# Performance work log

Measured on AMD Instinct MI355X. Metric: run time of the kernel, lower is better.

## Reference

```python
import jax, jax.numpy as jnp
import numpy as np
from jax import lax

B, C_IN, L = 16, 2, 8192
D, H, NL = 256, 8, 4
DK = D // H
DFF = 2 * D
S = L // 8  # downsampled length = 1024
EPS = 1e-5


def _pe(seq, d):
    pos = jnp.arange(seq, dtype=jnp.float32)[:, None]
    div = jnp.exp(jnp.arange(0, d, 2, dtype=jnp.float32) * (-np.log(10000.0) / d))
    pe = jnp.zeros((seq, d), dtype=jnp.float32)
    pe = pe.at[:, 0::2].set(jnp.sin(pos * div))
    pe = pe.at[:, 1::2].set(jnp.cos(pos * div))
    return pe  # (seq, d)


def _layernorm(x, g, b):
    m = jnp.mean(x, axis=-1, keepdims=True)
    v = jnp.mean((x - m) ** 2, axis=-1, keepdims=True)
    return (x - m) * lax.rsqrt(v + EPS) * g + b


def setup_inputs() -> dict:
    key = jax.random.key(0)
    ks = jax.random.split(key, 20)
    sd = 0.02
    inp = {
        'x': jax.random.normal(ks[0], (B, C_IN, L), jnp.float32),
        'conv1_w': jax.random.normal(ks[1], (32, C_IN, 8), jnp.float32) * sd,
        'conv1_b': jnp.zeros((32,), jnp.float32),
        'conv2_w': jax.random.normal(ks[2], (D, 32, 4), jnp.float32) * sd,
        'conv2_b': jnp.zeros((D,), jnp.float32),
        'wq': jax.random.normal(ks[3], (NL, D, D), jnp.float32) * sd,
        'bq': jnp.zeros((NL, D), jnp.float32),
        'wk': jax.random.normal(ks[4], (NL, D, D), jnp.float32) * sd,
        'bk': jnp.zeros((NL, D), jnp.float32),
        'wv': jax.random.normal(ks[5], (NL, D, D), jnp.float32) * sd,
        'bv': jnp.zeros((NL, D), jnp.float32),
        'wo': jax.random.normal(ks[6], (NL, D, D), jnp.float32) * sd,
        'bo': jnp.zeros((NL, D), jnp.float32),
        'ln1_g': jnp.ones((NL, D), jnp.float32),
        'ln1_b': jnp.zeros((NL, D), jnp.float32),
        'ff_w1': jax.random.normal(ks[7], (NL, D, DFF), jnp.float32) * sd,
        'ff_b1': jnp.zeros((NL, DFF), jnp.float32),
        'ff_w2': jax.random.normal(ks[8], (NL, DFF, D), jnp.float32) * sd,
        'ff_b2': jnp.zeros((NL, D), jnp.float32),
        'ln2_g': jnp.ones((NL, D), jnp.float32),
        'ln2_b': jnp.zeros((NL, D), jnp.float32),
        'cls_w1': jax.random.normal(ks[9], (D, D // 2), jnp.float32) * sd,
        'cls_b1': jnp.zeros((D // 2,), jnp.float32),
        'cls_w2': jax.random.normal(ks[10], (D // 2, 1), jnp.float32) * sd,
        'cls_b2': jnp.zeros((1,), jnp.float32),
    }
    return inp


def reference(x, conv1_w, conv1_b, conv2_w, conv2_b,
              wq, bq, wk, bk, wv, bv, wo, bo,
              ln1_g, ln1_b, ff_w1, ff_b1, ff_w2, ff_b2, ln2_g, ln2_b,
              cls_w1, cls_b1, cls_w2, cls_b2):
    dn = ('NCH', 'OIH', 'NCH')
    # downsampler: conv(k8,s4,p2) -> relu -> conv(k4,s2,p1) -> relu
    h = lax.conv_general_dilated(x, conv1_w, (4,), [(2, 2)], dimension_numbers=dn)
    h = jax.nn.relu(h + conv1_b[None, :, None])
    h = lax.conv_general_dilated(h, conv2_w, (2,), [(1, 1)], dimension_numbers=dn)
    h = jax.nn.relu(h + conv2_b[None, :, None])
    h = h.transpose(0, 2, 1)  # (B, S, D)
    h = h + _pe(h.shape[1], D)[None]
    scale = 1.0 / np.sqrt(DK)
    for i in range(NL):
        # multi-head attention (explicit QK^T -> softmax -> V)
        q = (h @ wq[i] + bq[i]).reshape(B, S, H, DK)
        k = (h @ wk[i] + bk[i]).reshape(B, S, H, DK)
        v = (h @ wv[i] + bv[i]).reshape(B, S, H, DK)
        scores = jnp.einsum('bqhd,bkhd->bhqk', q, k) * scale
        attn = jax.nn.softmax(scores, axis=-1)
        ctx = jnp.einsum('bhqk,bkhd->bqhd', attn, v).reshape(B, S, D)
        h = _layernorm(h + ctx @ wo[i] + bo[i], ln1_g[i], ln1_b[i])
        ff = jax.nn.relu(h @ ff_w1[i] + ff_b1[i]) @ ff_w2[i] + ff_b2[i]
        h = _layernorm(h + ff, ln2_g[i], ln2_b[i])
    pooled = jnp.mean(h, axis=1)  # (B, D)
    logits = jax.nn.relu(pooled @ cls_w1 + cls_b1) @ cls_w2 + cls_b2
    return jax.nn.sigmoid(logits)  # (B, 1)
```

## Files before the change

### kernel.cpp

```cpp
#include <hip/hip_runtime.h>
#include <math.h>

typedef unsigned short u16;
typedef __attribute__((ext_vector_type(8))) short bf16x8;
typedef __attribute__((ext_vector_type(4))) float f32x4;
typedef __attribute__((ext_vector_type(16))) float f32x16;

#define B_ 16
#define L_ 8192
#define D_ 256
#define H_ 8
#define NL_ 4
#define DFF_ 512
#define S_ 1024
#define L1_ 2048
#define MROWS_ 16384

__device__ __forceinline__ u16 f2bf(float f) {
    unsigned u = __float_as_uint(f);
    unsigned r = (u + 0x7fffu + ((u >> 16) & 1u)) >> 16;
    return (u16)r;
}
__device__ __forceinline__ float fexp2(float x) {
    return __builtin_amdgcn_exp2f(x);
}
__device__ __forceinline__ unsigned cvtpk(float a, float b) {
    unsigned r;
    asm("v_cvt_pk_bf16_f32 %0, %1, %2" : "=v"(r) : "v"(a), "v"(b));
    return r;
}
__device__ __forceinline__ void pl32swap(unsigned& dst, unsigned& src) {
    asm volatile("v_permlane32_swap_b32 %0, %1" : "+v"(dst), "+v"(src));
}
__device__ __forceinline__ int swz16(int b) { return b ^ ((b >> 3) & 0x18); }

typedef __attribute__((address_space(1))) const void gvoid;
typedef __attribute__((address_space(3))) void lvoid;
__device__ __forceinline__ void gll16(const void* g, void* l) {
    __builtin_amdgcn_global_load_lds((gvoid*)g, (lvoid*)l, 16, 0, 0);
}
__device__ __forceinline__ void stage64(const u16* src, int ld, u16* lds, int tid) {
    gll16(src + (size_t)(tid >> 2) * ld + (tid & 3) * 8, lds + (tid >> 6) * 512);
}

__global__ __launch_bounds__(256) void conv1_im2col_kernel(const float* __restrict__ x,
                                                           const float* __restrict__ w,
                                                           const float* __restrict__ bias,
                                                           u16* __restrict__ A2) {
    int idx = blockIdx.x * 256 + threadIdx.x;
    int k = idx & 127, row = idx >> 7;
    int c = k >> 2, j = k & 3;
    int b = row >> 10, s = row & 1023;
    int p = s * 2 - 1 + j;
    float v = 0.f;
    if (p >= 0 && p < L1_) {
        float acc = bias[c];
        int base = p * 4 - 2;
#pragma unroll
        for (int ci = 0; ci < 2; ++ci) {
            const float* xr = x + ((size_t)(b * 2 + ci)) * L_;
            const float* wr = w + (c * 2 + ci) * 8;
#pragma unroll
            for (int jj = 0; jj < 8; ++jj) {
                int pos = base + jj;
                if (pos >= 0 && pos < L_) acc += xr[pos] * wr[jj];
            }
        }
        v = fmaxf(acc, 0.f);
    }
    A2[idx] = f2bf(v);
}

__global__ __launch_bounds__(256) void pack_all(const float* __restrict__ wq,
                                                const float* __restrict__ wk,
                                                const float* __restrict__ wv,
                                                const float* __restrict__ wo,
                                                const float* __restrict__ ff_w1,
                                                const float* __restrict__ ff_w2,
                                                const float* __restrict__ conv2_w,
                                                const float* __restrict__ bq,
                                                const float* __restrict__ bk,
                                                const float* __restrict__ bv,
                                                u16* __restrict__ qkvT, u16* __restrict__ woT,
                                                u16* __restrict__ ff1T, u16* __restrict__ ff2T,
                                                u16* __restrict__ w2cT,
                                                float* __restrict__ pe, float* __restrict__ bqkv,
                                                float* __restrict__ pooled, float qscale) {
    int id = blockIdx.x * 256 + threadIdx.x;
    if (id < 786432) {
        int l = id / 196608, j = id % 196608;
        int row = j >> 8, k = j & 255;
        const float* src; float sc = 1.f; int n;
        if (row < 256) { src = wq; n = row; sc = qscale; }
        else if (row < 512) { src = wk; n = row - 256; }
        else { src = wv; n = row - 512; }
        qkvT[id] = f2bf(src[((size_t)l * 256 + k) * 256 + n] * sc);
        return;
    }
    id -= 786432;
    if (id < 262144) {
        int l = id >> 16, j = id & 65535;
        int n = j >> 8, k = j & 255;
        woT[id] = f2bf(wo[((size_t)l * 256 + k) * 256 + n]);
        return;
    }
    id -= 262144;
    if (id < 524288) {
        int l = id >> 17, j = id & 131071;
        int n = j >> 8, k = j & 255;
        ff1T[id] = f2bf(ff_w1[((size_t)l * 256 + k) * 512 + n]);
        return;
    }
    id -= 524288;
    if (id < 524288) {
        int l = id >> 17, j = id & 131071;
        int n = j >> 9, k = j & 511;
        ff2T[id] = f2bf(ff_w2[((size_t)l * 512 + k) * 256 + n]);
        return;
    }
    id -= 524288;
    if (id < 32768) { w2cT[id] = f2bf(conv2_w[id]); return; }
    id -= 32768;
    if (id < 262144) {
        int s = id >> 8, d = id & 255;
        int i2 = d & ~1;
        float div = expf((float)i2 * (-9.210340371976184f / 256.f));
        float arg = (float)s * div;
        pe[id] = (d & 1) ? cosf(arg) : sinf(arg);
        return;
    }
    id -= 262144;
    if (id < 3072) {
        int l = id / 768, n = id % 768;
        const float* src = (n < 256) ? bq : (n < 512) ? bk : bv;
        float sc = (n < 256) ? qscale : 1.f;
        bqkv[id] = src[l * 256 + (n & 255)] * sc;
        return;
    }
    id -= 3072;
    if (id < 4096) pooled[id] = 0.f;
}

template <int EP>
__global__ __launch_bounds__(256) void mfma_gemm128(const u16* __restrict__ A, int lda,
                                                    const u16* __restrict__ WT,
                                                    const float* __restrict__ bias,
                                                    const float* __restrict__ pe,
                                                    float* __restrict__ hout,
                                                    u16* __restrict__ outB,
                                                    u16* __restrict__ ktout,
                                                    u16* __restrict__ vtout,
                                                    int N, int K) {
    __shared__ u16 Alds[128 * 32];
    __shared__ u16 Blds[128 * 32];
    int tid = threadIdx.x;
    int lane = tid & 63, w = tid >> 6;
    int lo = lane & 15, hi = lane >> 4;
    int m0 = blockIdx.y * 128;
    int n0 = blockIdx.x * 128;
    int wm = (w >> 1) * 64, wn = (w & 1) * 64;
    f32x4 acc[4][4];
#pragma unroll
    for (int i = 0; i < 4; ++i)
#pragma unroll
        for (int j = 0; j < 4; ++j) acc[i][j] = (f32x4){0.f, 0.f, 0.f, 0.f};

    for (int k0 = 0; k0 < K; k0 += 32) {
        stage64(A + (size_t)m0 * lda + k0, lda, Alds, tid);
        stage64(A + (size_t)(m0 + 64) * lda + k0, lda, Alds + 2048, tid);
        stage64(WT + (size_t)n0 * K + k0, K, Blds, tid);
        stage64(WT + (size_t)(n0 + 64) * K + k0, K, Blds + 2048, tid);
        __syncthreads();
        bf16x8 af[4], bfr[4];
#pragma unroll
        for (int mf = 0; mf < 4; ++mf) af[mf] = *(bf16x8*)&Alds[(wm + mf * 16 + lo) * 32 + hi * 8];
#pragma unroll
        for (int nf = 0; nf < 4; ++nf) bfr[nf] = *(bf16x8*)&Blds[(wn + nf * 16 + lo) * 32 + hi * 8];
#pragma unroll
        for (int mf = 0; mf < 4; ++mf)
#pragma unroll
            for (int nf = 0; nf < 4; ++nf)
                acc[mf][nf] = __builtin_amdgcn_mfma_f32_16x16x32_bf16(af[mf], bfr[nf], acc[mf][nf], 0, 0, 0);
        __syncthreads();
    }
#pragma unroll
    for (int mf = 0; mf < 4; ++mf)
#pragma unroll
        for (int nf = 0; nf < 4; ++nf) {
            int col = n0 + wn + nf * 16 + lo;
            float bb = bias[col];
            int rowb = m0 + wm + mf * 16 + hi * 4;
            if (EP == 3 && col >= 512) {
                int dc = col - 512;
                int bhh = ((rowb >> 10) << 3) + (dc >> 5);
                int s = rowb & 1023;
                unsigned u0 = (unsigned)f2bf(acc[mf][nf][0] + bb) |
                              ((unsigned)f2bf(acc[mf][nf][1] + bb) << 16);
                unsigned u1 = (unsigned)f2bf(acc[mf][nf][2] + bb) |
                              ((unsigned)f2bf(acc[mf][nf][3] + bb) << 16);
                uint2 val = {u0, u1};
                *(uint2*)(vtout + (((size_t)bhh * 32 + (s >> 5)) * 32 + (dc & 31)) * 32 + (s & 31)) = val;
            } else if (EP == 3 && col >= 256) {
                int kc = col - 256;
                int bhh = ((rowb >> 10) << 3) + (kc >> 5);
                int s = rowb & 1023;
                u16* kt_base = ktout + (((size_t)bhh * 32 + (s >> 5)) * 32) * 32;
#pragma unroll
                for (int r = 0; r < 4; ++r)
                    kt_base[((s & 31) + r) * 32 + (kc & 31)] = f2bf(acc[mf][nf][r] + bb);
            } else {
#pragma unroll
                for (int r = 0; r < 4; ++r) {
                    float v = acc[mf][nf][r] + bb;
                    if (EP == 2) v = fmaxf(v, 0.f);
                    if (EP == 2) {
                        v += pe[((rowb + r) & 1023) * 256 + col];
                        hout[(size_t)(rowb + r) * 256 + col] = v;
                        outB[(size_t)(rowb + r) * 256 + col] = f2bf(v);
                    } else {
                        outB[(size_t)(rowb + r) * 256 + col] = f2bf(v);
                    }
                }
            }
        }
}

__global__ __launch_bounds__(256) void mfma_gemm_ln(const u16* __restrict__ A, int lda,
                                                    const u16* __restrict__ WT,
                                                    const float* __restrict__ bias,
                                                    const float* __restrict__ resid,
                                                    const float* __restrict__ g,
                                                    const float* __restrict__ b2,
                                                    float* __restrict__ hout,
                                                    u16* __restrict__ hbout,
                                                    int K) {
    __shared__ u16 Alds[32 * 32];
    __shared__ u16 Blds[256 * 32];
    __shared__ float red1[32][4];
    __shared__ float red2[32][4];
    int tid = threadIdx.x;
    int lane = tid & 63, w = tid >> 6;
    int lo = lane & 15, hi = lane >> 4;
    int m0 = blockIdx.x * 32;
    int wn = w * 64;
    f32x4 acc[2][4];
#pragma unroll
    for (int i = 0; i < 2; ++i)
#pragma unroll
        for (int j = 0; j < 4; ++j) acc[i][j] = (f32x4){0.f, 0.f, 0.f, 0.f};

    for (int k0 = 0; k0 < K; k0 += 32) {
        if (tid < 128)
            gll16(A + (size_t)(m0 + (tid >> 2)) * lda + k0 + (tid & 3) * 8, Alds + (tid >> 6) * 512);
        stage64(WT + (size_t)0 * K + k0, K, Blds, tid);
        stage64(WT + (size_t)64 * K + k0, K, Blds + 2048, tid);
        stage64(WT + (size_t)128 * K + k0, K, Blds + 4096, tid);
        stage64(WT + (size_t)192 * K + k0, K, Blds + 6144, tid);
        __syncthreads();
        bf16x8 af[2], bfr[4];
#pragma unroll
        for (int mf = 0; mf < 2; ++mf) af[mf] = *(bf16x8*)&Alds[(mf * 16 + lo) * 32 + hi * 8];
#pragma unroll
        for (int nf = 0; nf < 4; ++nf) bfr[nf] = *(bf16x8*)&Blds[(wn + nf * 16 + lo) * 32 + hi * 8];
#pragma unroll
        for (int mf = 0; mf < 2; ++mf)
#pragma unroll
            for (int nf = 0; nf < 4; ++nf)
                acc[mf][nf] = __builtin_amdgcn_mfma_f32_16x16x32_bf16(af[mf], bfr[nf], acc[mf][nf], 0, 0, 0);
        __syncthreads();
    }

#pragma unroll
    for (int mf = 0; mf < 2; ++mf)
#pragma unroll
        for (int nf = 0; nf < 4; ++nf) {
            int col = wn + nf * 16 + lo;
            float bb = bias[col];
#pragma unroll
            for (int r = 0; r < 4; ++r) {
                int row = m0 + mf * 16 + hi * 4 + r;
                acc[mf][nf][r] += bb + resid[(size_t)row * 256 + col];
            }
        }
#pragma unroll
    for (int mf = 0; mf < 2; ++mf)
#pragma unroll
        for (int r = 0; r < 4; ++r) {
            float s1 = acc[mf][0][r] + acc[mf][1][r] + acc[mf][2][r] + acc[mf][3][r];
            float s2 = acc[mf][0][r] * acc[mf][0][r] + acc[mf][1][r] * acc[mf][1][r] +
                       acc[mf][2][r] * acc[mf][2][r] + acc[mf][3][r] * acc[mf][3][r];
#pragma unroll
            for (int off = 1; off < 16; off <<= 1) {
                s1 += __shfl_xor(s1, off);
                s2 += __shfl_xor(s2, off);
            }
            if (lo == 0) {
                red1[mf * 16 + hi * 4 + r][w] = s1;
                red2[mf * 16 + hi * 4 + r][w] = s2;
            }
        }
    __syncthreads();
#pragma unroll
    for (int mf = 0; mf < 2; ++mf)
#pragma unroll
        for (int r = 0; r < 4; ++r) {
            int rl = mf * 16 + hi * 4 + r;
            float mean = (red1[rl][0] + red1[rl][1] + red1[rl][2] + red1[rl][3]) * (1.f / 256.f);
            float e2 = (red2[rl][0] + red2[rl][1] + red2[rl][2] + red2[rl][3]) * (1.f / 256.f);
            float rs = rsqrtf(e2 - mean * mean + 1e-5f);
#pragma unroll
            for (int nf = 0; nf < 4; ++nf) {
                int col = wn + nf * 16 + lo;
                float o = (acc[mf][nf][r] - mean) * rs * g[col] + b2[col];
                hout[(size_t)(m0 + rl) * 256 + col] = o;
                hbout[(size_t)(m0 + rl) * 256 + col] = f2bf(o);
            }
        }
}

template <int LAST>
__global__ __launch_bounds__(256) void fused_ff(const u16* __restrict__ A,
                                                const u16* __restrict__ W1T,
                                                const float* __restrict__ b1,
                                                const u16* __restrict__ W2T,
                                                const float* __restrict__ b2,
                                                const float* __restrict__ resid,
                                                const float* __restrict__ g,
                                                const float* __restrict__ bln,
                                                float* __restrict__ hout,
                                                u16* __restrict__ hbout,
                                                float* __restrict__ pooled) {
    __shared__ char hid[16 * 2048];
    __shared__ float red1[32][4];
    __shared__ float red2[32][4];
    int tid = threadIdx.x;
    int lane = tid & 63, w = tid >> 6;
    int lo = lane & 15, hi = lane >> 4;
    int m0 = blockIdx.x * 32;

    {
        int wn = w * 128;
        f32x4 acc[2][8];
#pragma unroll
        for (int i = 0; i < 2; ++i)
#pragma unroll
            for (int j = 0; j < 8; ++j) acc[i][j] = (f32x4){0.f, 0.f, 0.f, 0.f};
        for (int k0 = 0; k0 < 256; k0 += 32) {
            bf16x8 af[2], bfr[8];
#pragma unroll
            for (int mf = 0; mf < 2; ++mf)
                af[mf] = *(const bf16x8*)(A + (size_t)(m0 + mf * 16 + lo) * 256 + k0 + hi * 8);
#pragma unroll
            for (int nf = 0; nf < 8; ++nf)
                bfr[nf] = *(const bf16x8*)(W1T + (size_t)(wn + nf * 16 + lo) * 256 + k0 + hi * 8);
#pragma unroll
            for (int mf = 0; mf < 2; ++mf)
#pragma unroll
                for (int nf = 0; nf < 8; ++nf)
                    acc[mf][nf] = __builtin_amdgcn_mfma_f32_16x16x32_bf16(af[mf], bfr[nf], acc[mf][nf], 0, 0, 0);
        }
#pragma unroll
        for (int mf = 0; mf < 2; ++mf)
#pragma unroll
            for (int nf = 0; nf < 8; ++nf) {
                int col = wn + nf * 16 + lo;
                float bb = b1[col];
                char* tile = hid + (col >> 5) * 2048;
                int c2 = (col & 31) * 2;
#pragma unroll
                for (int r = 0; r < 4; ++r) {
                    int row = mf * 16 + hi * 4 + r;
                    *(u16*)(tile + swz16(row * 64 + c2)) = f2bf(fmaxf(acc[mf][nf][r] + bb, 0.f));
                }
            }
    }
    __syncthreads();

    int wn = w * 64;
    f32x4 acc[2][4];
#pragma unroll
    for (int i = 0; i < 2; ++i)
#pragma unroll
        for (int j = 0; j < 4; ++j) acc[i][j] = (f32x4){0.f, 0.f, 0.f, 0.f};
    for (int k0 = 0; k0 < 512; k0 += 32) {
        bf16x8 af[2], bfr[4];
        const char* tile = hid + (k0 >> 5) * 2048;
#pragma unroll
        for (int mf = 0; mf < 2; ++mf)
            af[mf] = *(const bf16x8*)(tile + swz16((mf * 16 + lo) * 64 + hi * 16));
#pragma unroll
        for (int nf = 0; nf < 4; ++nf)
            bfr[nf] = *(const bf16x8*)(W2T + (size_t)(wn + nf * 16 + lo) * 512 + k0 + hi * 8);
#pragma unroll
        for (int mf = 0; mf < 2; ++mf)
#pragma unroll
            for (int nf = 0; nf < 4; ++nf)
                acc[mf][nf] = __builtin_amdgcn_mfma_f32_16x16x32_bf16(af[mf], bfr[nf], acc[mf][nf], 0, 0, 0);
    }

#pragma unroll
    for (int mf = 0; mf < 2; ++mf)
#pragma unroll
        for (int nf = 0; nf < 4; ++nf) {
            int col = wn + nf * 16 + lo;
            float bb = b2[col];
#pragma unroll
            for (int r = 0; r < 4; ++r) {
                int row = m0 + mf * 16 + hi * 4 + r;
                acc[mf][nf][r] += bb + resid[(size_t)row * 256 + col];
            }
        }
#pragma unroll
    for (int mf = 0; mf < 2; ++mf)
#pragma unroll
        for (int r = 0; r < 4; ++r) {
            float s1 = acc[mf][0][r] + acc[mf][1][r] + acc[mf][2][r] + acc[mf][3][r];
            float s2 = acc[mf][0][r] * acc[mf][0][r] + acc[mf][1][r] * acc[mf][1][r] +
                       acc[mf][2][r] * acc[mf][2][r] + acc[mf][3][r] * acc[mf][3][r];
#pragma unroll
            for (int off = 1; off < 16; off <<= 1) {
                s1 += __shfl_xor(s1, off);
                s2 += __shfl_xor(s2, off);
            }
            if (lo == 0) {
                red1[mf * 16 + hi * 4 + r][w] = s1;
                red2[mf * 16 + hi * 4 + r][w] = s2;
            }
        }
    __syncthreads();
    float colsum[4] = {0.f, 0.f, 0.f, 0.f};
#pragma unroll
    for (int mf = 0; mf < 2; ++mf)
#pragma unroll
        for (int r = 0; r < 4; ++r) {
            int rl = mf * 16 + hi * 4 + r;
            float mean = (red1[rl][0] + red1[rl][1] + red1[rl][2] + red1[rl][3]) * (1.f / 256.f);
            float e2 = (red2[rl][0] + red2[rl][1] + red2[rl][2] + red2[rl][3]) * (1.f / 256.f);
            float rs = rsqrtf(e2 - mean * mean + 1e-5f);
#pragma unroll
            for (int nf = 0; nf < 4; ++nf) {
                int col = wn + nf * 16 + lo;
                float o = (acc[mf][nf][r] - mean) * rs * g[col] + bln[col];
                if (LAST) {
                    colsum[nf] += o;
                } else {
                    hout[(size_t)(m0 + rl) * 256 + col] = o;
                    hbout[(size_t)(m0 + rl) * 256 + col] = f2bf(o);
                }
            }
        }
    if (LAST) {
        int b = m0 >> 10;
#pragma unroll
        for (int nf = 0; nf < 4; ++nf) {
            float cs = colsum[nf];
            cs += __shfl_xor(cs, 16);
            cs += __shfl_xor(cs, 32);
            if (hi == 0) atomicAdd(&pooled[b * 256 + wn + nf * 16 + lo], cs);
        }
    }
}

__global__ __launch_bounds__(256) void attn_mfma(u16* __restrict__ qbuf,
                                                 const u16* __restrict__ ktiles,
                                                 const u16* __restrict__ vtiles) {
    int tid = threadIdx.x;
    int lane = tid & 63, w = tid >> 6;
    int q = lane & 31, h = lane >> 5;
    int phys = blockIdx.x;
    int bid = (phys & 7) * 128 + (phys >> 3);
    int qt = bid & 7, hh = (bid >> 3) & 7, bb = bid >> 6;
    int q0 = qt * 128 + w * 32;
    size_t rowbase = (size_t)bb * S_;

    const u16* qrow = qbuf + (rowbase + q0 + q) * 256 + hh * 32;
    bf16x8 qf0 = *(const bf16x8*)(qrow + h * 8);
    bf16x8 qf1 = *(const bf16x8*)(qrow + 16 + h * 8);

    const u16* kb = ktiles + (size_t)(bb * 8 + hh) * 32768 + q * 32 + h * 8;
    const u16* vb = vtiles + (size_t)(bb * 8 + hh) * 32768 + q * 32 + h * 8;

    f32x16 O = {0.f, 0.f, 0.f, 0.f, 0.f, 0.f, 0.f, 0.f, 0.f, 0.f, 0.f, 0.f, 0.f, 0.f, 0.f, 0.f};
    float l = 0.f;

#define LOADT(d0, d1, d2, d3, t)                         \
    {                                                    \
        const u16* kr = kb + (t) * 1024;                 \
        d0 = *(const bf16x8*)kr;                         \
        d1 = *(const bf16x8*)(kr + 16);                  \
        const u16* vr = vb + (t) * 1024;                 \
        d2 = *(const bf16x8*)vr;                         \
        d3 = *(const bf16x8*)(vr + 16);                  \
    }

#define TILE_BODY(kf0_, kf1_, vf0_, vf1_)                                               \
    {                                                                                   \
        f32x16 S = {0.f, 0.f, 0.f, 0.f, 0.f, 0.f, 0.f, 0.f,                             \
                    0.f, 0.f, 0.f, 0.f, 0.f, 0.f, 0.f, 0.f};                            \
        __builtin_amdgcn_s_setprio(1);                                                  \
        S = __builtin_amdgcn_mfma_f32_32x32x16_bf16(kf0_, qf0, S, 0, 0, 0);             \
        S = __builtin_amdgcn_mfma_f32_32x32x16_bf16(kf1_, qf1, S, 0, 0, 0);             \
        __builtin_amdgcn_s_setprio(0);                                                  \
        _Pragma("unroll") for (int i = 0; i < 16; ++i) S[i] = fexp2(S[i]);              \
        float t0 = (S[0] + S[1]) + (S[2] + S[3]);                                       \
        float t1 = (S[4] + S[5]) + (S[6] + S[7]);                                       \
        float t2 = (S[8] + S[9]) + (S[10] + S[11]);                                     \
        float t3 = (S[12] + S[13]) + (S[14] + S[15]);                                   \
        float ls = (t0 + t1) + (t2 + t3);                                               \
        unsigned ua = __float_as_uint(ls), ub = ua;                                     \
        pl32swap(ua, ub);                                                               \
        l += __uint_as_float(ua) + __uint_as_float(ub);                                 \
        unsigned pk[8];                                                                 \
        _Pragma("unroll") for (int i = 0; i < 8; ++i) pk[i] = cvtpk(S[2 * i], S[2 * i + 1]); \
        pl32swap(pk[2], pk[0]);                                                         \
        pl32swap(pk[3], pk[1]);                                                         \
        pl32swap(pk[6], pk[4]);                                                         \
        pl32swap(pk[7], pk[5]);                                                         \
        uint4 t4 = {pk[0], pk[1], pk[2], pk[3]};                                        \
        uint4 t5 = {pk[4], pk[5], pk[6], pk[7]};                                        \
        bf16x8 pf0 = *(bf16x8*)&t4;                                                     \
        bf16x8 pf1 = *(bf16x8*)&t5;                                                     \
        __builtin_amdgcn_s_setprio(1);                                                  \
        O = __builtin_amdgcn_mfma_f32_32x32x16_bf16(vf0_, pf0, O, 0, 0, 0);             \
        O = __builtin_amdgcn_mfma_f32_32x32x16_bf16(vf1_, pf1, O, 0, 0, 0);             \
        __builtin_amdgcn_s_setprio(0);                                                  \
    }

    bf16x8 ka0, ka1, va0, va1, kb0, kb1, vb0, vb1;
    LOADT(ka0, ka1, va0, va1, 0);
    LOADT(kb0, kb1, vb0, vb1, 1);
    for (int kt = 0; kt < 32; kt += 2) {
        bf16x8 kc0 = ka0, kc1 = ka1, vc0 = va0, vc1 = va1;
        if (kt + 2 < 32) LOADT(kc0, kc1, vc0, vc1, kt + 2);
        TILE_BODY(ka0, ka1, va0, va1);
        bf16x8 kd0 = kb0, kd1 = kb1, vd0 = vb0, vd1 = vb1;
        if (kt + 3 < 32) LOADT(kd0, kd1, vd0, vd1, kt + 3);
        TILE_BODY(kb0, kb1, vb0, vb1);
        ka0 = kc0; ka1 = kc1; va0 = vc0; va1 = vc1;
        kb0 = kd0; kb1 = kd1; vb0 = vd0; vb1 = vd1;
    }
#undef LOADT
#undef TILE_BODY

    float inv = 1.f / l;
    u16* orow = qbuf + (rowbase + q0 + q) * 256 + hh * 32;
#pragma unroll
    for (int gg = 0; gg < 4; ++gg) {
        unsigned u0 = cvtpk(O[4 * gg] * inv, O[4 * gg + 1] * inv);
        unsigned u1 = cvtpk(O[4 * gg + 2] * inv, O[4 * gg + 3] * inv);
        uint2 val = {u0, u1};
        *(uint2*)(orow + gg * 8 + h * 4) = val;
    }
}

__global__ __launch_bounds__(256) void cls_kernel(const float* __restrict__ pooled,
                                                  const float* __restrict__ w1,
                                                  const float* __restrict__ b1,
                                                  const float* __restrict__ w2,
                                                  const float* __restrict__ b2,
                                                  float* __restrict__ out) {
    int b = blockIdx.x;
    int d = threadIdx.x;
    __shared__ float pl[256];
    __shared__ float hid[128];
    pl[d] = pooled[b * 256 + d] * (1.f / 1024.f);
    __syncthreads();
    if (d < 128) {
        float a = b1[d];
        for (int k = 0; k < 256; ++k) a += pl[k] * w1[k * 128 + d];
        hid[d] = fmaxf(a, 0.f);
    }
    __syncthreads();
    if (d == 0) {
        float a = b2[0];
        for (int k = 0; k < 128; ++k) a += hid[k] * w2[k];
        out[b] = 1.f / (1.f + expf(-a));
    }
}

extern "C" void kernel_launch(void* const* d_in, const int* in_sizes, int n_in,
                              void* d_out, int out_size, void* d_ws, size_t ws_size,
                              hipStream_t stream) {
    const float* x       = (const float*)d_in[0];
    const float* conv1_w = (const float*)d_in[1];
    const float* conv1_b = (const float*)d_in[2];
    const float* conv2_w = (const float*)d_in[3];
    const float* conv2_b = (const float*)d_in[4];
    const float* wq      = (const float*)d_in[5];
    const float* bq      = (const float*)d_in[6];
    const float* wk      = (const float*)d_in[7];
    const float* bk      = (const float*)d_in[8];
    const float* wv      = (const float*)d_in[9];
    const float* bv      = (const float*)d_in[10];
    const float* wo      = (const float*)d_in[11];
    const float* bo      = (const float*)d_in[12];
    const float* ln1_g   = (const float*)d_in[13];
    const float* ln1_b   = (const float*)d_in[14];
    const float* ff_w1   = (const float*)d_in[15];
    const float* ff_b1   = (const float*)d_in[16];
    const float* ff_w2   = (const float*)d_in[17];
    const float* ff_b2   = (const float*)d_in[18];
    const float* ln2_g   = (const float*)d_in[19];
    const float* ln2_b   = (const float*)d_in[20];
    const float* cls_w1  = (const float*)d_in[21];
    const float* cls_b1  = (const float*)d_in[22];
    const float* cls_w2  = (const float*)d_in[23];
    const float* cls_b2  = (const float*)d_in[24];

    char* wsb = (char*)d_ws;
    float* h    = (float*)wsb;
    u16*   hb   = (u16*)(wsb + ((size_t)16 << 20));
    u16*   qbuf = (u16*)(wsb + ((size_t)24 << 20));
    u16*   ktl  = (u16*)(wsb + ((size_t)32 << 20));
    u16*   vtl  = (u16*)(wsb + ((size_t)40 << 20));
    u16*   A2   = (u16*)(wsb + ((size_t)32 << 20));
    float* pe   = (float*)(wsb + ((size_t)48 << 20));
    char*  pkb  = wsb + ((size_t)49 << 20);
    u16*   qkvT = (u16*)pkb;
    u16*   woT  = qkvT + (size_t)4 * 768 * 256;
    u16*   ff1T = woT + (size_t)4 * 256 * 256;
    u16*   ff2T = ff1T + (size_t)4 * 512 * 256;
    u16*   w2cT = ff2T + (size_t)4 * 512 * 256;
    float* bqkv = (float*)(w2cT + 256 * 128);
    float* pooled = bqkv + 4 * 768;

    const float qscale = 0.17677669529663687f * 1.4426950408889634f;
    pack_all<<<9372, 256, 0, stream>>>(wq, wk, wv, wo, ff_w1, ff_w2, conv2_w, bq, bk, bv,
                                       qkvT, woT, ff1T, ff2T, w2cT, pe, bqkv, pooled, qscale);

    conv1_im2col_kernel<<<8192, 256, 0, stream>>>(x, conv1_w, conv1_b, A2);
    mfma_gemm128<2><<<dim3(2, 128), 256, 0, stream>>>(A2, 128, w2cT, conv2_b, pe, h, hb,
                                                      nullptr, nullptr, 256, 128);

    for (int l = 0; l < NL_; ++l) {
        const u16* qkvT_l = qkvT + (size_t)l * 768 * 256;
        const u16* woT_l  = woT + (size_t)l * 256 * 256;
        const u16* ff1T_l = ff1T + (size_t)l * 512 * 256;
        const u16* ff2T_l = ff2T + (size_t)l * 256 * 512;

        mfma_gemm128<3><<<dim3(6, 128), 256, 0, stream>>>(hb, 256, qkvT_l, bqkv + l * 768,
                                                          nullptr, nullptr, qbuf, ktl, vtl, 256, 256);
        attn_mfma<<<1024, 256, 0, stream>>>(qbuf, ktl, vtl);
        mfma_gemm_ln<<<512, 256, 0, stream>>>(qbuf, 256, woT_l, bo + l * 256, h,
                                              ln1_g + l * 256, ln1_b + l * 256, h, hb, 256);
        if (l < NL_ - 1) {
            fused_ff<0><<<512, 256, 0, stream>>>(hb, ff1T_l, ff_b1 + l * 512, ff2T_l,
                                                 ff_b2 + l * 256, h, ln2_g + l * 256,
                                                 ln2_b + l * 256, h, hb, nullptr);
        } else {
            fused_ff<1><<<512, 256, 0, stream>>>(hb, ff1T_l, ff_b1 + l * 512, ff2T_l,
                                                 ff_b2 + l * 256, h, ln2_g + l * 256,
                                                 ln2_b + l * 256, h, hb, pooled);
        }
    }

    cls_kernel<<<B_, 256, 0, stream>>>(pooled, cls_w1, cls_b1, cls_w2, cls_b2, (float*)d_out);
}
```

Measured before the change: 598.6 us.

## Remap blocks to XCDs for locality and stage FFN weights through LDS

Grid indices in the GEMM, GEMM+LN and fused FFN kernels are remapped so that consecutive row tiles land on the same XCD (blockIdx & 7). The aim is better L2 reuse of the shared weights and adjacent activations. The fused FFN kernel now loads W1/W2 and A tiles into LDS with global_load_lds and synchronises each k-step, instead of reading directly from global memory per wave. The hidden buffer switches to an XOR-swizzled row-major layout. LDS use grows considerably (32KB B plus 32KB hidden), which may reduce occupancy, and the extra barriers add synchronisation cost.

```diff
diff --git a/kernel.cpp b/kernel.cpp
--- a/kernel.cpp
+++ b/kernel.cpp
@@ -32,7 +32,6 @@
 __device__ __forceinline__ void pl32swap(unsigned& dst, unsigned& src) {
     asm volatile("v_permlane32_swap_b32 %0, %1" : "+v"(dst), "+v"(src));
 }
-__device__ __forceinline__ int swz16(int b) { return b ^ ((b >> 3) & 0x18); }
 
 typedef __attribute__((address_space(1))) const void gvoid;
 typedef __attribute__((address_space(3))) void lvoid;
@@ -141,7 +140,7 @@
     if (id < 4096) pooled[id] = 0.f;
 }
 
-template <int EP>
+template <int EP, int NT>
 __global__ __launch_bounds__(256) void mfma_gemm128(const u16* __restrict__ A, int lda,
                                                     const u16* __restrict__ WT,
                                                     const float* __restrict__ bias,
@@ -156,8 +155,10 @@
     int tid = threadIdx.x;
     int lane = tid & 63, w = tid >> 6;
     int lo = lane & 15, hi = lane >> 4;
-    int m0 = blockIdx.y * 128;
-    int n0 = blockIdx.x * 128;
+    int phys = blockIdx.x;
+    int cid = phys & 7, idx = phys >> 3;
+    int m0 = (cid * 16 + idx / NT) * 128;
+    int n0 = (idx % NT) * 128;
     int wm = (w >> 1) * 64, wn = (w & 1) * 64;
     f32x4 acc[4][4];
 #pragma unroll
@@ -241,7 +242,8 @@
     int tid = threadIdx.x;
     int lane = tid & 63, w = tid >> 6;
     int lo = lane & 15, hi = lane >> 4;
-    int m0 = blockIdx.x * 32;
+    int phys = blockIdx.x;
+    int m0 = ((phys & 7) * 64 + (phys >> 3)) * 32;
     int wn = w * 64;
     f32x4 acc[2][4];
 #pragma unroll
@@ -330,34 +332,42 @@
                                                 float* __restrict__ hout,
                                                 u16* __restrict__ hbout,
                                                 float* __restrict__ pooled) {
-    __shared__ char hid[16 * 2048];
+    __shared__ u16 Blds[512 * 32];
+    __shared__ u16 Alds[32 * 32];
+    __shared__ u16 hid[32 * 512];
     __shared__ float red1[32][4];
     __shared__ float red2[32][4];
     int tid = threadIdx.x;
     int lane = tid & 63, w = tid >> 6;
     int lo = lane & 15, hi = lane >> 4;
-    int m0 = blockIdx.x * 32;
+    int phys = blockIdx.x;
+    int m0 = ((phys & 7) * 64 + (phys >> 3)) * 32;
 
     {
         int wn = w * 128;
-        f32x4 acc[2][8];
+        f32x4 acc1[2][8];
 #pragma unroll
         for (int i = 0; i < 2; ++i)
 #pragma unroll
-            for (int j = 0; j < 8; ++j) acc[i][j] = (f32x4){0.f, 0.f, 0.f, 0.f};
+            for (int j = 0; j < 8; ++j) acc1[i][j] = (f32x4){0.f, 0.f, 0.f, 0.f};
         for (int k0 = 0; k0 < 256; k0 += 32) {
+            if (tid < 128)
+                gll16(A + (size_t)(m0 + (tid >> 2)) * 256 + k0 + (tid & 3) * 8, Alds + (tid >> 6) * 512);
+#pragma unroll
+            for (int rr = 0; rr < 8; ++rr)
+                stage64(W1T + (size_t)(rr * 64) * 256 + k0, 256, Blds + rr * 2048, tid);
+            __syncthreads();
             bf16x8 af[2], bfr[8];
 #pragma unroll
+            for (int mf = 0; mf < 2; ++mf) af[mf] = *(bf16x8*)&Alds[(mf * 16 + lo) * 32 + hi * 8];
+#pragma unroll
+            for (int nf = 0; nf < 8; ++nf) bfr[nf] = *(bf16x8*)&Blds[(wn + nf * 16 + lo) * 32 + hi * 8];
+#pragma unroll
             for (int mf = 0; mf < 2; ++mf)
-                af[mf] = *(const bf16x8*)(A + (size_t)(m0 + mf * 16 + lo) * 256 + k0 + hi * 8);
-#pragma unroll
-            for (int nf = 0; nf < 8; ++nf)
-                bfr[nf] = *(const bf16x8*)(W1T + (size_t)(wn + nf * 16 + lo) * 256 + k0 + hi * 8);
-#pragma unroll
-            for (int mf = 0; mf < 2; ++mf)
 #pragma unroll
                 for (int nf = 0; nf < 8; ++nf)
-                    acc[mf][nf] = __builtin_amdgcn_mfma_f32_16x16x32_bf16(af[mf], bfr[nf], acc[mf][nf], 0, 0, 0);
+                    acc1[mf][nf] = __builtin_amdgcn_mfma_f32_16x16x32_bf16(af[mf], bfr[nf], acc1[mf][nf], 0, 0, 0);
+            __syncthreads();
         }
 #pragma unroll
         for (int mf = 0; mf < 2; ++mf)
@@ -365,12 +375,10 @@
             for (int nf = 0; nf < 8; ++nf) {
                 int col = wn + nf * 16 + lo;
                 float bb = b1[col];
-                char* tile = hid + (col >> 5) * 2048;
-                int c2 = (col & 31) * 2;
 #pragma unroll
                 for (int r = 0; r < 4; ++r) {
-                    int row = mf * 16 + hi * 4 + r;
-                    *(u16*)(tile + swz16(row * 64 + c2)) = f2bf(fmaxf(acc[mf][nf][r] + bb, 0.f));
+                    int m = mf * 16 + hi * 4 + r;
+                    hid[(m * 512 + col) ^ ((m & 7) << 3)] = f2bf(fmaxf(acc1[mf][nf][r] + bb, 0.f));
                 }
             }
     }
@@ -383,19 +391,24 @@
 #pragma unroll
         for (int j = 0; j < 4; ++j) acc[i][j] = (f32x4){0.f, 0.f, 0.f, 0.f};
     for (int k0 = 0; k0 < 512; k0 += 32) {
+#pragma unroll
+        for (int rr = 0; rr < 4; ++rr)
+            stage64(W2T + (size_t)(rr * 64) * 512 + k0, 512, Blds + rr * 2048, tid);
+        __syncthreads();
         bf16x8 af[2], bfr[4];
-        const char* tile = hid + (k0 >> 5) * 2048;
-#pragma unroll
-        for (int mf = 0; mf < 2; ++mf)
-            af[mf] = *(const bf16x8*)(tile + swz16((mf * 16 + lo) * 64 + hi * 16));
-#pragma unroll
-        for (int nf = 0; nf < 4; ++nf)
-            bfr[nf] = *(const bf16x8*)(W2T + (size_t)(wn + nf * 16 + lo) * 512 + k0 + hi * 8);
+#pragma unroll
+        for (int mf = 0; mf < 2; ++mf) {
+            int m = mf * 16 + lo;
+            af[mf] = *(bf16x8*)&hid[(m * 512 + k0 + hi * 8) ^ ((m & 7) << 3)];
+        }
+#pragma unroll
+        for (int nf = 0; nf < 4; ++nf) bfr[nf] = *(bf16x8*)&Blds[(wn + nf * 16 + lo) * 32 + hi * 8];
 #pragma unroll
         for (int mf = 0; mf < 2; ++mf)
 #pragma unroll
             for (int nf = 0; nf < 4; ++nf)
                 acc[mf][nf] = __builtin_amdgcn_mfma_f32_16x16x32_bf16(af[mf], bfr[nf], acc[mf][nf], 0, 0, 0);
+        __syncthreads();
     }
 
 #pragma unroll
@@ -629,8 +642,8 @@
                                        qkvT, woT, ff1T, ff2T, w2cT, pe, bqkv, pooled, qscale);
 
     conv1_im2col_kernel<<<8192, 256, 0, stream>>>(x, conv1_w, conv1_b, A2);
-    mfma_gemm128<2><<<dim3(2, 128), 256, 0, stream>>>(A2, 128, w2cT, conv2_b, pe, h, hb,
-                                                      nullptr, nullptr, 256, 128);
+    mfma_gemm128<2, 2><<<256, 256, 0, stream>>>(A2, 128, w2cT, conv2_b, pe, h, hb,
+                                                nullptr, nullptr, 256, 128);
 
     for (int l = 0; l < NL_; ++l) {
         const u16* qkvT_l = qkvT + (size_t)l * 768 * 256;
@@ -638,8 +651,8 @@
         const u16* ff1T_l = ff1T + (size_t)l * 512 * 256;
         const u16* ff2T_l = ff2T + (size_t)l * 256 * 512;
 
-        mfma_gemm128<3><<<dim3(6, 128), 256, 0, stream>>>(hb, 256, qkvT_l, bqkv + l * 768,
-                                                          nullptr, nullptr, qbuf, ktl, vtl, 256, 256);
+        mfma_gemm128<3, 6><<<768, 256, 0, stream>>>(hb, 256, qkvT_l, bqkv + l * 768,
+                                                    nullptr, nullptr, qbuf, ktl, vtl, 256, 256);
         attn_mfma<<<1024, 256, 0, stream>>>(qbuf, ktl, vtl);
         mfma_gemm_ln<<<512, 256, 0, stream>>>(qbuf, 256, woT_l, bo + l * 256, h,
                                               ln1_g + l * 256, ln1_b + l * 256, h, hb, 256);
```

New measurement: 529.3 us. 1.13x faster.
